# Optimization experiments

Measured on AMD Instinct MI355X. Metric: run time of the kernel, lower is better.

Reference implementation:

```python
import jax, jax.numpy as jnp
import numpy as np

E, T, H, I = 16, 4, 512, 1024  # expert_num, task_num, hidden_size, input_size
B = 8192


def setup_inputs() -> dict:
    key = jax.random.key(0)
    ks = jax.random.split(key, 8)
    s_i = 1.0 / np.sqrt(I)
    s_h = 1.0 / np.sqrt(H)
    return {
        "x": jax.random.normal(ks[0], (B, I), dtype=jnp.float32),
        "We": jax.random.uniform(ks[1], (E, H, I), jnp.float32, -s_i, s_i),
        "be": jax.random.uniform(ks[2], (E, H), jnp.float32, -s_i, s_i),
        "Wg": jax.random.uniform(ks[3], (T, E, I), jnp.float32, -s_i, s_i),
        "bg": jax.random.uniform(ks[4], (T, E), jnp.float32, -s_i, s_i),
        "Wf": jax.random.uniform(ks[5], (T, H), jnp.float32, -s_h, s_h),
        "bf": jax.random.uniform(ks[6], (T,), jnp.float32, -s_h, s_h),
    }


def reference(x, We, be, Wg, bg, Wf, bf):
    # expert outputs: relu(x @ We_e^T + be_e)  -> [B, E, H]
    eo = jax.nn.relu(jnp.einsum("bi,ehi->beh", x, We) + be[None])
    # gate outputs: softmax over experts        -> [B, T, E]
    g = jax.nn.softmax(jnp.einsum("bi,tei->bte", x, Wg) + bg[None], axis=-1)
    # gated combine                             -> [T, B, H]
    res = jnp.einsum("bte,beh->tbh", g, eo)
    # per-task scalar heads                     -> [T, B, 1]
    out = jnp.einsum("tbh,th->tb", res, Wf) + bf[:, None]
    return out[:, :, None]
```

## Files before the change

kernel.cpp:

```cpp
#include <hip/hip_runtime.h>
#include <hip/hip_bf16.h>
#include <stdint.h>


#define E_ 16
#define T_ 4
#define H_ 512
#define I_ 1024
#define B_ 8192
#define N_ (E_ * H_)
#define K_ I_

typedef __bf16 bf16x8 __attribute__((ext_vector_type(8)));
typedef float f32x4 __attribute__((ext_vector_type(4)));

__device__ __forceinline__ unsigned short f2bf_rne(float f) {
  unsigned int b = __float_as_uint(f);
  b += 0x7fffu + ((b >> 16) & 1u);
  return (unsigned short)(b >> 16);
}

#define N4X (B_ * K_ / 4)
#define N4W (N_ * K_ / 4)
#define N4G (64 * K_ / 4)

__global__ __launch_bounds__(256) void cvt3_kernel(const float* __restrict__ x,
                                                   const float* __restrict__ We,
                                                   const float* __restrict__ Wg,
                                                   const float* __restrict__ bfv,
                                                   unsigned short* __restrict__ xb,
                                                   unsigned short* __restrict__ wb,
                                                   unsigned short* __restrict__ wgb,
                                                   float* __restrict__ out) {
  int i = blockIdx.x * 256 + threadIdx.x;
  if (i < T_ * B_) out[i] = bfv[i >> 13];
  const float* src;
  unsigned short* dst;
  int j;
  if (i < N4X) {
    src = x; dst = xb; j = i;
  } else if (i < N4X + N4W) {
    src = We; dst = wb; j = i - N4X;
  } else if (i < N4X + N4W + N4G) {
    src = Wg; dst = wgb; j = i - (N4X + N4W);
  } else {
    return;
  }
  float4 v = reinterpret_cast<const float4*>(src)[j];
  ushort4 o;
  o.x = f2bf_rne(v.x);
  o.y = f2bf_rne(v.y);
  o.z = f2bf_rne(v.z);
  o.w = f2bf_rne(v.w);
  reinterpret_cast<ushort4*>(dst)[j] = o;
}

__device__ __forceinline__ void gld_lds16(const void* gp, void* lp) {
  __builtin_amdgcn_global_load_lds((const __attribute__((address_space(1))) void*)gp,
                                   (__attribute__((address_space(3))) void*)lp, 16, 0, 0);
}

__global__ __launch_bounds__(256) void logits_softmax_kernel(
    const unsigned short* __restrict__ A,
    const unsigned short* __restrict__ Bm,
    const float* __restrict__ bg,
    float* __restrict__ g)
{
  __shared__ struct {
    unsigned short A[128 * 32];
    unsigned short B[64 * 32];
  } st;

  const int tid = threadIdx.x;
  const int w = tid >> 6, l = tid & 63;
  const int m16 = l & 15, q = l >> 4;
  const size_t m0 = (size_t)blockIdx.x * 128;

  const int r0s = (w * 2 + 0) * 16 + (l >> 2);
  const int r1s = (w * 2 + 1) * 16 + (l >> 2);
  const int slot = l & 3;
  const int c0 = slot ^ ((r0s >> 1) & 3);
  const int c1 = slot ^ ((r1s >> 1) & 3);
  const size_t offA0 = (m0 + r0s) * K_ + c0 * 8;
  const size_t offA1 = (m0 + r1s) * K_ + c1 * 8;
  const int l0 = (w * 2 + 0) * 512;
  const int l1 = (w * 2 + 1) * 512;
  const int rBs = w * 16 + (l >> 2);
  const int cB = slot ^ ((rBs >> 1) & 3);
  const size_t offB = (size_t)rBs * K_ + cB * 8;
  const int lB = w * 512;

  const int arow = w * 32 + m16;
  const int sA = q ^ ((arow >> 1) & 3);
  const int sB = q ^ ((m16 >> 1) & 3);

  f32x4 acc[2][4] = {};

  for (int k0 = 0; k0 < K_; k0 += 32) {
    __syncthreads();
    gld_lds16(A + offA0 + k0, st.A + l0);
    gld_lds16(A + offA1 + k0, st.A + l1);
    gld_lds16(Bm + offB + k0, st.B + lB);
    __syncthreads();
    bf16x8 af[2], bfr[4];
#pragma unroll
    for (int i = 0; i < 2; ++i)
      af[i] = *reinterpret_cast<const bf16x8*>(st.A + (arow + i * 16) * 32 + sA * 8);
#pragma unroll
    for (int j = 0; j < 4; ++j)
      bfr[j] = *reinterpret_cast<const bf16x8*>(st.B + (j * 16 + m16) * 32 + sB * 8);
#pragma unroll
    for (int i = 0; i < 2; ++i)
#pragma unroll
      for (int j = 0; j < 4; ++j)
        acc[i][j] = __builtin_amdgcn_mfma_f32_16x16x32_bf16(af[i], bfr[j], acc[i][j], 0, 0, 0);
  }

  float bgv[4];
#pragma unroll
  for (int j = 0; j < 4; ++j) bgv[j] = bg[j * 16 + m16];

#pragma unroll
  for (int i = 0; i < 2; ++i) {
    float lg[4][4];
#pragma unroll
    for (int j = 0; j < 4; ++j)
#pragma unroll
      for (int r = 0; r < 4; ++r) lg[r][j] = acc[i][j][r] + bgv[j];
#pragma unroll
    for (int r = 0; r < 4; ++r) {
#pragma unroll
      for (int j = 0; j < 4; ++j) {
        float m = lg[r][j];
#pragma unroll
        for (int mask = 1; mask < 16; mask <<= 1) m = fmaxf(m, __shfl_xor(m, mask, 64));
        float ex = __expf(lg[r][j] - m);
        float s = ex;
#pragma unroll
        for (int mask = 1; mask < 16; mask <<= 1) s += __shfl_xor(s, mask, 64);
        size_t b = m0 + w * 32 + i * 16 + q * 4 + r;
        g[b * 64 + j * 16 + m16] = ex / s;
      }
    }
  }
}

__global__ __launch_bounds__(256, 2) void moe_main_kernel(
    const unsigned short* __restrict__ A,
    const unsigned short* __restrict__ Bm,
    const float* __restrict__ be,
    const float* __restrict__ Wf,
    const float* __restrict__ g,
    float* __restrict__ out)
{
  __shared__ union {
    struct {
      unsigned short A0[128 * 32];
      unsigned short A1[128 * 32];
      unsigned short B0[128 * 32];
      unsigned short B1[128 * 32];
    } st;
    float allsums[2 * 512];
  } sm;

  const int tid = threadIdx.x;
  const int w = tid >> 6, l = tid & 63;
  const int wm = w >> 1, wn = w & 1;
  const int m16 = l & 15, q = l >> 4;
  const int mb = blockIdx.x, nb = blockIdx.y;
  const size_t m0 = (size_t)mb * 128, n0 = (size_t)nb * 128;

  const int r0s = (w * 2 + 0) * 16 + (l >> 2);
  const int r1s = (w * 2 + 1) * 16 + (l >> 2);
  const int slot = l & 3;
  const int c0 = slot ^ ((r0s >> 1) & 3);
  const int c1 = slot ^ ((r1s >> 1) & 3);
  const size_t offA0 = (m0 + r0s) * K_ + c0 * 8;
  const size_t offA1 = (m0 + r1s) * K_ + c1 * 8;
  const size_t offB0 = (n0 + r0s) * K_ + c0 * 8;
  const size_t offB1 = (n0 + r1s) * K_ + c1 * 8;
  const int l0 = (w * 2 + 0) * 512;
  const int l1 = (w * 2 + 1) * 512;

  const int arow = wm * 64 + m16;
  const int brow = wn * 64 + m16;
  const int sA = q ^ ((arow >> 1) & 3);
  const int sB = q ^ ((brow >> 1) & 3);

  f32x4 acc[4][4] = {};

  for (int k0 = 0; k0 < K_; k0 += 64) {
    __syncthreads();
    gld_lds16(A + offA0 + k0, sm.st.A0 + l0);
    gld_lds16(A + offA1 + k0, sm.st.A0 + l1);
    gld_lds16(A + offA0 + k0 + 32, sm.st.A1 + l0);
    gld_lds16(A + offA1 + k0 + 32, sm.st.A1 + l1);
    gld_lds16(Bm + offB0 + k0, sm.st.B0 + l0);
    gld_lds16(Bm + offB1 + k0, sm.st.B0 + l1);
    gld_lds16(Bm + offB0 + k0 + 32, sm.st.B1 + l0);
    gld_lds16(Bm + offB1 + k0 + 32, sm.st.B1 + l1);
    __syncthreads();
#pragma unroll
    for (int h = 0; h < 2; ++h) {
      const unsigned short* bufA = h ? sm.st.A1 : sm.st.A0;
      const unsigned short* bufB = h ? sm.st.B1 : sm.st.B0;
      bf16x8 af[4], bfr[4];
#pragma unroll
      for (int i = 0; i < 4; ++i)
        af[i] = *reinterpret_cast<const bf16x8*>(bufA + (arow + i * 16) * 32 + sA * 8);
#pragma unroll
      for (int j = 0; j < 4; ++j)
        bfr[j] = *reinterpret_cast<const bf16x8*>(bufB + (brow + j * 16) * 32 + sB * 8);
#pragma unroll
      for (int i = 0; i < 4; ++i)
#pragma unroll
        for (int j = 0; j < 4; ++j)
          acc[i][j] = __builtin_amdgcn_mfma_f32_16x16x32_bf16(af[i], bfr[j], acc[i][j], 0, 0, 0);
    }
  }

  __syncthreads();

  const int hbase = (int)(n0 & 511);

  float wfv[4][4];
#pragma unroll
  for (int t = 0; t < 4; ++t)
#pragma unroll
    for (int j = 0; j < 4; ++j)
      wfv[t][j] = Wf[t * H_ + hbase + wn * 64 + j * 16 + m16];
  float bias[4];
#pragma unroll
  for (int j = 0; j < 4; ++j) bias[j] = be[n0 + wn * 64 + j * 16 + m16];

  const int b0s = m16 & 1, b1s = (m16 >> 1) & 1, b2s = (m16 >> 2) & 1, b3s = (m16 >> 3) & 1;
#pragma unroll
  for (int i = 0; i < 4; ++i) {
    float eo[4][4];
#pragma unroll
    for (int j = 0; j < 4; ++j)
#pragma unroll
      for (int r = 0; r < 4; ++r) eo[j][r] = fmaxf(acc[i][j][r] + bias[j], 0.f);
    float p[16];
#pragma unroll
    for (int r = 0; r < 4; ++r)
#pragma unroll
      for (int t = 0; t < 4; ++t) {
        float v = 0.f;
#pragma unroll
        for (int j = 0; j < 4; ++j) v += eo[j][r] * wfv[t][j];
        p[r * 4 + t] = v;
      }
    float q8[8];
#pragma unroll
    for (int m = 0; m < 8; ++m) {
      float sent = b0s ? p[2 * m] : p[2 * m + 1];
      float recv = __shfl_xor(sent, 1, 64);
      q8[m] = (b0s ? p[2 * m + 1] : p[2 * m]) + recv;
    }
    float q4[4];
#pragma unroll
    for (int u = 0; u < 4; ++u) {
      float sent = b1s ? q8[2 * u] : q8[2 * u + 1];
      float recv = __shfl_xor(sent, 2, 64);
      q4[u] = (b1s ? q8[2 * u + 1] : q8[2 * u]) + recv;
    }
    float q2[2];
#pragma unroll
    for (int u = 0; u < 2; ++u) {
      float sent = b2s ? q4[2 * u] : q4[2 * u + 1];
      float recv = __shfl_xor(sent, 4, 64);
      q2[u] = (b2s ? q4[2 * u + 1] : q4[2 * u]) + recv;
    }
    float sent = b3s ? q2[0] : q2[1];
    float recv = __shfl_xor(sent, 8, 64);
    float v = (b3s ? q2[1] : q2[0]) + recv;

    int row = wm * 64 + i * 16 + q * 4 + (m16 >> 2);
    sm.allsums[wn * 512 + row * 4 + (m16 & 3)] = v;
  }
  __syncthreads();

  const int e_idx = (int)(n0 >> 9);
#pragma unroll
  for (int oi = 0; oi < 2; ++oi) {
    int o = tid * 2 + oi;
    int row = o >> 2, t = o & 3;
    float s = sm.allsums[row * 4 + t] + sm.allsums[512 + row * 4 + t];
    size_t b = m0 + row;
    float gv = g[b * 64 + t * 16 + e_idx];
    atomicAdd(&out[(size_t)t * B_ + b], gv * s);
  }
}

extern "C" void kernel_launch(void* const* d_in, const int* in_sizes, int n_in,
                              void* d_out, int out_size, void* d_ws, size_t ws_size,
                              hipStream_t stream) {
  const float* x = (const float*)d_in[0];
  const float* We = (const float*)d_in[1];
  const float* be = (const float*)d_in[2];
  const float* Wg = (const float*)d_in[3];
  const float* bg = (const float*)d_in[4];
  const float* Wf = (const float*)d_in[5];
  const float* bf = (const float*)d_in[6];
  float* out = (float*)d_out;

  unsigned short* xb = (unsigned short*)d_ws;
  unsigned short* wb = xb + (size_t)B_ * K_;
  unsigned short* wgb = wb + (size_t)N_ * K_;
  float* g = (float*)(wgb + (size_t)64 * K_);

  cvt3_kernel<<<(N4X + N4W + N4G + 255) / 256, 256, 0, stream>>>(x, We, Wg, bf, xb, wb, wgb, out);
  logits_softmax_kernel<<<B_ / 128, 256, 0, stream>>>(xb, wgb, bg, g);
  dim3 grid(B_ / 128, N_ / 128);
  moe_main_kernel<<<grid, 256, 0, stream>>>(xb, wb, be, Wf, g, out);
}
```

Measured before the change: 263.8 us.

## Rewrite main GEMM as 256x256 tile, 8-wave, double-buffered pipelined kernel

The main MoE GEMM kernel moves from 128x128 tiles with 4 waves and a synchronous load-then-compute loop to 256x256 tiles with 8 waves. The new loop uses 128KB of dynamic LDS with two buffers, interleaves the global-to-LDS loads for the next K slice with the MFMA work on the current one, and raises wave priority around the MFMAs. The epilogue now reduces across 4 N-waves instead of 2. This is meant to raise data reuse per loaded byte and hide memory latency behind MFMA work. The cost is a large LDS footprint and high register pressure, which limits occupancy, and many extra barriers.

```diff
diff --git a/kernel.cpp b/kernel.cpp
--- a/kernel.cpp
+++ b/kernel.cpp
@@ -145,7 +145,64 @@
   }
 }
 
-__global__ __launch_bounds__(256, 2) void moe_main_kernel(
+
+extern __shared__ char smem[];
+
+#define BARRIER()                          \
+  do {                                     \
+    asm volatile("" ::: "memory");         \
+    __builtin_amdgcn_s_barrier();          \
+    asm volatile("" ::: "memory");         \
+  } while (0)
+#define VMW(n) asm volatile("s_waitcnt vmcnt(" #n ")" ::: "memory")
+
+#define STAGE_A(d, h, kk)                                                              \
+  do {                                                                                 \
+    gld_lds16(A + baseAg + (h)*131072 + (kk), smem + (d)*65536 + (h)*16384 + ldsW);    \
+    gld_lds16(A + baseAg + (h)*131072 + 8192 + (kk),                                   \
+              smem + (d)*65536 + (h)*16384 + ldsW + 1024);                             \
+  } while (0)
+#define STAGE_B(d, h, kk)                                                              \
+  do {                                                                                 \
+    gld_lds16(Bm + baseBg + (h)*131072 + (kk),                                         \
+              smem + (d)*65536 + 32768 + (h)*16384 + ldsW);                            \
+    gld_lds16(Bm + baseBg + (h)*131072 + 8192 + (kk),                                  \
+              smem + (d)*65536 + 32768 + (h)*16384 + ldsW + 1024);                     \
+  } while (0)
+
+#define LDA4(d, ib)                                                                       \
+  do {                                                                                    \
+    _Pragma("unroll") for (int i2 = 0; i2 < 4; ++i2) {                                    \
+      af[i2][0] = *reinterpret_cast<const bf16x8*>(smem + (d)*65536 + baseA_rd +          \
+                                                   ((ib) + i2) * 2048 + slK0);            \
+      af[i2][1] = *reinterpret_cast<const bf16x8*>(smem + (d)*65536 + baseA_rd +          \
+                                                   ((ib) + i2) * 2048 + slK1);            \
+    }                                                                                     \
+  } while (0)
+#define LDB2(d, jb)                                                                       \
+  do {                                                                                    \
+    _Pragma("unroll") for (int j2 = 0; j2 < 2; ++j2) {                                    \
+      bfr[(jb) + j2][0] = *reinterpret_cast<const bf16x8*>(smem + (d)*65536 + baseB_rd +  \
+                                                           ((jb) + j2) * 2048 + slK0);    \
+      bfr[(jb) + j2][1] = *reinterpret_cast<const bf16x8*>(smem + (d)*65536 + baseB_rd +  \
+                                                           ((jb) + j2) * 2048 + slK1);    \
+    }                                                                                     \
+  } while (0)
+
+#define MFMAQ(ib, jb)                                                                     \
+  do {                                                                                    \
+    __builtin_amdgcn_s_setprio(1);                                                        \
+    _Pragma("unroll") for (int i2 = 0; i2 < 4; ++i2)                                      \
+        _Pragma("unroll") for (int j2 = 0; j2 < 2; ++j2) {                                \
+      acc[(ib) + i2][(jb) + j2] = __builtin_amdgcn_mfma_f32_16x16x32_bf16(                \
+          af[i2][0], bfr[(jb) + j2][0], acc[(ib) + i2][(jb) + j2], 0, 0, 0);              \
+      acc[(ib) + i2][(jb) + j2] = __builtin_amdgcn_mfma_f32_16x16x32_bf16(                \
+          af[i2][1], bfr[(jb) + j2][1], acc[(ib) + i2][(jb) + j2], 0, 0, 0);              \
+    }                                                                                     \
+    __builtin_amdgcn_s_setprio(0);                                                        \
+  } while (0)
+
+__global__ __launch_bounds__(512, 2) void moe_main_kernel(
     const unsigned short* __restrict__ A,
     const unsigned short* __restrict__ Bm,
     const float* __restrict__ be,
@@ -153,89 +210,91 @@
     const float* __restrict__ g,
     float* __restrict__ out)
 {
-  __shared__ union {
-    struct {
-      unsigned short A0[128 * 32];
-      unsigned short A1[128 * 32];
-      unsigned short B0[128 * 32];
-      unsigned short B1[128 * 32];
-    } st;
-    float allsums[2 * 512];
-  } sm;
-
   const int tid = threadIdx.x;
   const int w = tid >> 6, l = tid & 63;
-  const int wm = w >> 1, wn = w & 1;
+  const int wm = w >> 2, wn = w & 3;
   const int m16 = l & 15, q = l >> 4;
   const int mb = blockIdx.x, nb = blockIdx.y;
-  const size_t m0 = (size_t)mb * 128, n0 = (size_t)nb * 128;
-
-  const int r0s = (w * 2 + 0) * 16 + (l >> 2);
-  const int r1s = (w * 2 + 1) * 16 + (l >> 2);
-  const int slot = l & 3;
-  const int c0 = slot ^ ((r0s >> 1) & 3);
-  const int c1 = slot ^ ((r1s >> 1) & 3);
-  const size_t offA0 = (m0 + r0s) * K_ + c0 * 8;
-  const size_t offA1 = (m0 + r1s) * K_ + c1 * 8;
-  const size_t offB0 = (n0 + r0s) * K_ + c0 * 8;
-  const size_t offB1 = (n0 + r1s) * K_ + c1 * 8;
-  const int l0 = (w * 2 + 0) * 512;
-  const int l1 = (w * 2 + 1) * 512;
-
-  const int arow = wm * 64 + m16;
-  const int brow = wn * 64 + m16;
-  const int sA = q ^ ((arow >> 1) & 3);
-  const int sB = q ^ ((brow >> 1) & 3);
-
-  f32x4 acc[4][4] = {};
-
-  for (int k0 = 0; k0 < K_; k0 += 64) {
-    __syncthreads();
-    gld_lds16(A + offA0 + k0, sm.st.A0 + l0);
-    gld_lds16(A + offA1 + k0, sm.st.A0 + l1);
-    gld_lds16(A + offA0 + k0 + 32, sm.st.A1 + l0);
-    gld_lds16(A + offA1 + k0 + 32, sm.st.A1 + l1);
-    gld_lds16(Bm + offB0 + k0, sm.st.B0 + l0);
-    gld_lds16(Bm + offB1 + k0, sm.st.B0 + l1);
-    gld_lds16(Bm + offB0 + k0 + 32, sm.st.B1 + l0);
-    gld_lds16(Bm + offB1 + k0 + 32, sm.st.B1 + l1);
-    __syncthreads();
-#pragma unroll
-    for (int h = 0; h < 2; ++h) {
-      const unsigned short* bufA = h ? sm.st.A1 : sm.st.A0;
-      const unsigned short* bufB = h ? sm.st.B1 : sm.st.B0;
-      bf16x8 af[4], bfr[4];
-#pragma unroll
-      for (int i = 0; i < 4; ++i)
-        af[i] = *reinterpret_cast<const bf16x8*>(bufA + (arow + i * 16) * 32 + sA * 8);
-#pragma unroll
-      for (int j = 0; j < 4; ++j)
-        bfr[j] = *reinterpret_cast<const bf16x8*>(bufB + (brow + j * 16) * 32 + sB * 8);
-#pragma unroll
-      for (int i = 0; i < 4; ++i)
-#pragma unroll
-        for (int j = 0; j < 4; ++j)
-          acc[i][j] = __builtin_amdgcn_mfma_f32_16x16x32_bf16(af[i], bfr[j], acc[i][j], 0, 0, 0);
-    }
-  }
-
-  __syncthreads();
-
-  const int hbase = (int)(n0 & 511);
+  const size_t m0 = (size_t)mb * 256, n0 = (size_t)nb * 256;
+
+  const size_t baseAg = (m0 + w * 16 + (l >> 3)) * K_ + (size_t)(((l & 7) ^ (l >> 3)) * 8);
+  const size_t baseBg = (n0 + w * 16 + (l >> 3)) * K_ + (size_t)(((l & 7) ^ (l >> 3)) * 8);
+  const int ldsW = w * 2048;
+
+  const int slK0 = ((q) ^ (m16 & 7)) * 16;
+  const int slK1 = ((4 + q) ^ (m16 & 7)) * 16;
+  const int baseA_rd = (wm * 128 + m16) * 128;
+  const int baseB_rd = 32768 + (wn * 64 + m16) * 128;
+
+  f32x4 acc[8][4] = {};
+  bf16x8 af[4][2], bfr[4][2];
+
+  STAGE_A(0, 0, 0);
+  STAGE_A(0, 1, 0);
+  STAGE_B(0, 0, 0);
+  STAGE_B(0, 1, 0);
+  STAGE_B(1, 0, 64);
+  STAGE_B(1, 1, 64);
+  VMW(4);
+  BARRIER();
+
+#pragma unroll 1
+  for (int n = 0; n < 7; ++n) {
+    const int kA1 = (2 * n + 1) * 64;
+    const int kN2 = (2 * n + 2) * 64;
+    const int kB3 = (2 * n + 3) * 64;
+    LDA4(0, 0); LDB2(0, 0); STAGE_A(1, 0, kA1);
+    BARRIER(); MFMAQ(0, 0); BARRIER();
+    LDB2(0, 2); STAGE_A(1, 1, kA1);
+    BARRIER(); MFMAQ(0, 2); BARRIER();
+    LDA4(0, 4); STAGE_B(0, 0, kN2);
+    BARRIER(); MFMAQ(4, 2); BARRIER();
+    STAGE_B(0, 1, kN2); VMW(4);
+    BARRIER(); MFMAQ(4, 0); BARRIER();
+    LDA4(1, 0); LDB2(1, 0); STAGE_A(0, 0, kN2);
+    BARRIER(); MFMAQ(0, 0); BARRIER();
+    LDB2(1, 2); STAGE_A(0, 1, kN2);
+    BARRIER(); MFMAQ(0, 2); BARRIER();
+    LDA4(1, 4); STAGE_B(1, 0, kB3);
+    BARRIER(); MFMAQ(4, 2); BARRIER();
+    STAGE_B(1, 1, kB3); VMW(4);
+    BARRIER(); MFMAQ(4, 0); BARRIER();
+  }
+
+  LDA4(0, 0); LDB2(0, 0); STAGE_A(1, 0, 15 * 64);
+  BARRIER(); MFMAQ(0, 0); BARRIER();
+  LDB2(0, 2); STAGE_A(1, 1, 15 * 64);
+  BARRIER(); MFMAQ(0, 2); BARRIER();
+  LDA4(0, 4);
+  BARRIER(); MFMAQ(4, 2); BARRIER();
+  VMW(0);
+  BARRIER(); MFMAQ(4, 0); BARRIER();
+  LDA4(1, 0); LDB2(1, 0);
+  BARRIER(); MFMAQ(0, 0); BARRIER();
+  LDB2(1, 2);
+  BARRIER(); MFMAQ(0, 2); BARRIER();
+  LDA4(1, 4);
+  BARRIER(); MFMAQ(4, 2); BARRIER();
+  MFMAQ(4, 0);
+
+  float* allsums = (float*)smem;
+
+  const int hb = (int)(n0 & 511);
+  const int e_idx = (int)(n0 >> 9);
 
   float wfv[4][4];
 #pragma unroll
   for (int t = 0; t < 4; ++t)
 #pragma unroll
     for (int j = 0; j < 4; ++j)
-      wfv[t][j] = Wf[t * H_ + hbase + wn * 64 + j * 16 + m16];
+      wfv[t][j] = Wf[t * H_ + hb + wn * 64 + j * 16 + m16];
   float bias[4];
 #pragma unroll
   for (int j = 0; j < 4; ++j) bias[j] = be[n0 + wn * 64 + j * 16 + m16];
 
   const int b0s = m16 & 1, b1s = (m16 >> 1) & 1, b2s = (m16 >> 2) & 1, b3s = (m16 >> 3) & 1;
 #pragma unroll
-  for (int i = 0; i < 4; ++i) {
+  for (int i = 0; i < 8; ++i) {
     float eo[4][4];
 #pragma unroll
     for (int j = 0; j < 4; ++j)
@@ -276,20 +335,27 @@
     float recv = __shfl_xor(sent, 8, 64);
     float v = (b3s ? q2[1] : q2[0]) + recv;
 
-    int row = wm * 64 + i * 16 + q * 4 + (m16 >> 2);
-    sm.allsums[wn * 512 + row * 4 + (m16 & 3)] = v;
+    int row = wm * 128 + i * 16 + q * 4 + (m16 >> 2);
+    allsums[wn * 1024 + row * 4 + (m16 & 3)] = v;
   }
   __syncthreads();
 
-  const int e_idx = (int)(n0 >> 9);
-#pragma unroll
-  for (int oi = 0; oi < 2; ++oi) {
-    int o = tid * 2 + oi;
-    int row = o >> 2, t = o & 3;
-    float s = sm.allsums[row * 4 + t] + sm.allsums[512 + row * 4 + t];
-    size_t b = m0 + row;
-    float gv = g[b * 64 + t * 16 + e_idx];
-    atomicAdd(&out[(size_t)t * B_ + b], gv * s);
+  {
+    float2 s = *reinterpret_cast<float2*>(&allsums[0 * 1024 + tid * 2]);
+    float2 x1 = *reinterpret_cast<float2*>(&allsums[1 * 1024 + tid * 2]);
+    float2 x2 = *reinterpret_cast<float2*>(&allsums[2 * 1024 + tid * 2]);
+    float2 x3 = *reinterpret_cast<float2*>(&allsums[3 * 1024 + tid * 2]);
+    s.x += x1.x + x2.x + x3.x;
+    s.y += x1.y + x2.y + x3.y;
+#pragma unroll
+    for (int oi = 0; oi < 2; ++oi) {
+      int o = tid * 2 + oi;
+      int row = o >> 2, t = o & 3;
+      float sv = oi ? s.y : s.x;
+      size_t b = m0 + row;
+      float gv = g[b * 64 + t * 16 + e_idx];
+      atomicAdd(&out[(size_t)t * B_ + b], gv * sv);
+    }
   }
 }
 
@@ -310,8 +376,11 @@
   unsigned short* wgb = wb + (size_t)N_ * K_;
   float* g = (float*)(wgb + (size_t)64 * K_);
 
+  hipFuncSetAttribute((const void*)moe_main_kernel,
+                      hipFuncAttributeMaxDynamicSharedMemorySize, 131072);
+
   cvt3_kernel<<<(N4X + N4W + N4G + 255) / 256, 256, 0, stream>>>(x, We, Wg, bf, xb, wb, wgb, out);
   logits_softmax_kernel<<<B_ / 128, 256, 0, stream>>>(xb, wgb, bg, g);
-  dim3 grid(B_ / 128, N_ / 128);
-  moe_main_kernel<<<grid, 256, 0, stream>>>(xb, wb, be, Wf, g, out);
-}
+  dim3 grid(B_ / 256, N_ / 256);
+  moe_main_kernel<<<grid, 512, 131072, stream>>>(xb, wb, be, Wf, g, out);
+}
```

After: 250.3 us. 1.05x faster.
